# Kernel optimization log

Measured on AMD Instinct MI355X. Metric: run time of the kernel, lower is better.

The kernel has to match this reference:

```python
import jax, jax.numpy as jnp
from jax import lax
import numpy as np

CHANNEL_N = 16
HIDDEN = 128
INPUT_CH = 1
KSIZE = 7
STEPS = 10
EPS = 1e-5


def setup_inputs() -> dict:
    key = jax.random.key(0)
    ks = jax.random.split(key, 8)
    B, H, W = 8, 256, 256
    x = jax.random.normal(ks[0], (B, H, W, CHANNEL_N), dtype=jnp.float32)
    # stochastic fire masks, one per step (torch: bernoulli_(p=fire_rate) under no_grad)
    masks = jax.random.bernoulli(ks[1], 0.5, (STEPS, B, 1, H, W))
    # depthwise conv: groups=channel_n -> weight [C,1,K,K]
    conv_w = jax.random.normal(ks[2], (CHANNEL_N, 1, KSIZE, KSIZE), dtype=jnp.float32) * 0.05
    conv_b = jax.random.normal(ks[3], (CHANNEL_N,), dtype=jnp.float32) * 0.05
    # fc0: 1x1 conv [hidden, 2*C]
    fc0_w = jax.random.normal(ks[4], (HIDDEN, 2 * CHANNEL_N), dtype=jnp.float32) * 0.1
    fc0_b = jax.random.normal(ks[5], (HIDDEN,), dtype=jnp.float32) * 0.05
    # fc1: 1x1 conv [C - input_channels, hidden], no bias (zero-init in torch; random here)
    fc1_w = jax.random.normal(ks[6], (CHANNEL_N - INPUT_CH, HIDDEN), dtype=jnp.float32) * 0.02
    bn_gamma = jnp.ones((HIDDEN,), dtype=jnp.float32)
    bn_beta = jnp.zeros((HIDDEN,), dtype=jnp.float32)
    return {"x": x, "masks": masks, "conv_w": conv_w, "conv_b": conv_b,
            "fc0_w": fc0_w, "fc0_b": fc0_b, "fc1_w": fc1_w,
            "bn_gamma": bn_gamma, "bn_beta": bn_beta}


def _nca_forward(x, masks, conv_w, conv_b, fc0_w, fc0_b, fc1_w, bn_gamma, bn_beta):
    state = jnp.transpose(x, (0, 3, 1, 2))  # b h w c -> b c h w
    const_in = state[:, :INPUT_CH]
    pad = (KSIZE - 1) // 2

    def step(state, mask):
        # depthwise 7x7 conv, reflect padding
        sp = jnp.pad(state, ((0, 0), (0, 0), (pad, pad), (pad, pad)), mode='reflect')
        d = lax.conv_general_dilated(
            sp, conv_w, window_strides=(1, 1), padding='VALID',
            dimension_numbers=('NCHW', 'OIHW', 'NCHW'),
            feature_group_count=CHANNEL_N)
        d = d + conv_b[None, :, None, None]
        cat = jnp.concatenate([state, d], axis=1)  # [B, 2C, H, W]
        # fc0 (1x1 conv)
        h = jnp.einsum('bchw,oc->bohw', cat, fc0_w) + fc0_b[None, :, None, None]
        # BatchNorm2d with batch statistics (track_running_stats=False)
        mean = jnp.mean(h, axis=(0, 2, 3), keepdims=True)
        var = jnp.var(h, axis=(0, 2, 3), keepdims=True)
        h = (h - mean) * lax.rsqrt(var + EPS)
        h = h * bn_gamma[None, :, None, None] + bn_beta[None, :, None, None]
        h = jax.nn.relu(h)
        # fc1 (1x1 conv, no bias)
        delta = jnp.einsum('bohw,ko->bkhw', h, fc1_w)  # [B, C-1, H, W]
        delta = delta * mask  # stochastic fire (broadcast over channels)
        new = state[:, INPUT_CH:] + delta
        return jnp.concatenate([const_in, new], axis=1), None

    state, _ = lax.scan(step, state, masks.astype(state.dtype))
    return jnp.transpose(state, (0, 2, 3, 1))  # b c h w -> b h w c


def reference(x, masks, conv_w, conv_b, fc0_w, fc0_b, fc1_w, bn_gamma, bn_beta):
    return _nca_forward(x, masks, conv_w, conv_b, fc0_w, fc0_b, fc1_w, bn_gamma, bn_beta)
```

## Files before the change

kernel.cpp:

```cpp
#include <hip/hip_runtime.h>

#define CH 16
#define HID 128
#define NB 8
#define NH 256
#define NW 256
#define NPX (NB*NH*NW)
#define NSTEP 10
#define STEPSTATS 2240
#define GPW 8
#define KPW 4
#define SLAB 1280

typedef __attribute__((ext_vector_type(8))) short short8v;
typedef __attribute__((ext_vector_type(4))) float f32x4;

__device__ __forceinline__ int refl(int i, int n){
    if (i < 0) i = -i;
    if (i >= n) i = 2*n - 2 - i;
    return i;
}

__device__ __forceinline__ unsigned short f2bf(float x){
    unsigned int u = __float_as_uint(x);
    u += 0x7FFFu + ((u >> 16) & 1u);
    return (unsigned short)(u >> 16);
}
__device__ __forceinline__ float bf2f(unsigned short h){
    return __uint_as_float(((unsigned int)h) << 16);
}
__device__ __forceinline__ unsigned int cvtpk(float lo, float hi){
    unsigned int r;
    asm("v_cvt_pk_bf16_f32 %0, %1, %2" : "=v"(r) : "v"(lo), "v"(hi));
    return r;
}

__global__ void k_repack(const float* __restrict__ cw, const float* __restrict__ w0,
                         float* __restrict__ wp,
                         unsigned short* __restrict__ b0h, unsigned short* __restrict__ b0l){
    int t = blockIdx.x*256 + threadIdx.x;
    if (t < 49*16){ int tap = t >> 4, c = t & 15; wp[tap*16 + c] = cw[c*49 + tap]; }
    if (t < 4096){
        int n = t >> 9, l = (t >> 3) & 63, i = t & 7;
        int o = 16*n + (l & 15), k = ((l >> 4) << 3) + i;
        float v = w0[o*32 + k];
        unsigned short hi = f2bf(v);
        b0h[t] = hi;
        b0l[t] = f2bf(v - bf2f(hi));
    }
}

__global__ void k_zero(float* __restrict__ p, int n){
    int t = blockIdx.x*256 + threadIdx.x;
    if (t < n) p[t] = 0.f;
}

struct Row { float4 e[4]; float4 o[4]; };

__device__ __forceinline__ void fma4(float4& a, float4 w, float4 v){
    a.x += w.x*v.x; a.y += w.y*v.y; a.z += w.z*v.z; a.w += w.w*v.w;
}
__device__ __forceinline__ void ldrow(Row& r, const float4* L, int row, int tx){
    #pragma unroll
    for (int k=0;k<4;++k){
        r.e[k] = L[(row*2+0)*20 + tx + k];
        r.o[k] = L[(row*2+1)*20 + tx + k];
    }
}

__global__ __launch_bounds__(256,3)
void k_conv(const float* __restrict__ st, const float* __restrict__ wp,
            const float* __restrict__ cb, float* __restrict__ dout){
    __shared__ float4 tile4[38*2*20];
    __shared__ float4 cw4s[49];
    const int b = blockIdx.z >> 2, cg = blockIdx.z & 3;
    const int y0 = blockIdx.y*32, x0 = blockIdx.x*32;
    const int t = threadIdx.x;
    const int tx = t & 15, ty = t >> 4;

    if (t < 49) cw4s[t] = *(const float4*)&wp[t*16 + cg*4];
    for (int i = t; i < 38*38; i += 256){
        int py = i / 38, px = i - py*38;
        int gy = refl(y0 + py - 3, NH);
        int gx = refl(x0 + px - 3, NW);
        float4 v = *(const float4*)&st[(((size_t)b*NH + gy)*NW + gx)*CH + cg*4];
        tile4[(py*2 + (px&1))*20 + (px>>1)] = v;
    }
    __syncthreads();

    const float4* L = tile4;
    float4 bias = *(const float4*)&cb[cg*4];
    float4 a00 = bias, a01 = bias, a10 = bias, a11 = bias;
    Row A, B;
    ldrow(A, L, 2*ty,   tx);
    ldrow(B, L, 2*ty+1, tx);

#define CSTEP(dy, RA, RB, LOADNEXT, NR) \
    { \
        _Pragma("unroll") \
        for (int dx = 0; dx < 7; ++dx){ \
            float4 w4 = cw4s[(dy)*7 + dx]; \
            float4 v00 = ((dx)&1)   ? RA.o[(dx)>>1]   : RA.e[(dx)>>1]; \
            float4 v01 = ((dx+1)&1) ? RA.o[(dx+1)>>1] : RA.e[(dx+1)>>1]; \
            float4 v10 = ((dx)&1)   ? RB.o[(dx)>>1]   : RB.e[(dx)>>1]; \
            float4 v11 = ((dx+1)&1) ? RB.o[(dx+1)>>1] : RB.e[(dx+1)>>1]; \
            fma4(a00,w4,v00); fma4(a01,w4,v01); fma4(a10,w4,v10); fma4(a11,w4,v11); \
        } \
        if (LOADNEXT) ldrow(RA, L, NR, tx); \
    }

    CSTEP(0, A, B, 1, 2*ty+2)
    CSTEP(1, B, A, 1, 2*ty+3)
    CSTEP(2, A, B, 1, 2*ty+4)
    CSTEP(3, B, A, 1, 2*ty+5)
    CSTEP(4, A, B, 1, 2*ty+6)
    CSTEP(5, B, A, 1, 2*ty+7)
    CSTEP(6, A, B, 0, 0)
#undef CSTEP

    const size_t pr = ((size_t)b*NH + (size_t)(y0 + 2*ty))*NW + (x0 + 2*tx);
    *(float4*)&dout[(pr)*CH + cg*4]        = a00;
    *(float4*)&dout[(pr+1)*CH + cg*4]      = a01;
    *(float4*)&dout[(pr+NW)*CH + cg*4]     = a10;
    *(float4*)&dout[(pr+NW+1)*CH + cg*4]   = a11;
}

__global__ __launch_bounds__(512)
void k_stats(const float* __restrict__ st, const float* __restrict__ dv,
             float* __restrict__ S){
    __shared__ float lds[8*SLAB];
    const int t = threadIdx.x, lane = t & 63, w = t >> 6;
    const int lo = lane & 15, hi = lane >> 4;
    float* slab = &lds[w*SLAB];
    const int gw = blockIdx.x*8 + w;

    short8v ones;
    {
        short ov = (lo == 0) ? (short)0x3F80 : (short)0;
        #pragma unroll
        for (int i=0;i<8;++i) ones[i] = ov;
    }
    f32x4 a00 = (f32x4){0.f,0.f,0.f,0.f};
    f32x4 a01 = a00, a11 = a00, s0 = a00, s1 = a00;

    const int lp = lane >> 3, lq = lane & 7;
    const float* lbase = (lq < 4) ? st : dv;
    const int lch = (lq & 3) * 4;
    const size_t p0 = (size_t)gw * (KPW*32);

    float4 v[4];
    #pragma unroll
    for (int j2=0;j2<4;++j2)
        v[j2] = *(const float4*)&lbase[(p0 + lp + 8*j2)*CH + lch];

    #pragma unroll
    for (int j=0;j<KPW;++j){
        #pragma unroll
        for (int j2=0;j2<4;++j2){
            int p = lp + 8*j2;
            *(float2*)&slab[p*34 + lq*4]     = make_float2(v[j2].x, v[j2].y);
            *(float2*)&slab[p*34 + lq*4 + 2] = make_float2(v[j2].z, v[j2].w);
        }
        if (j+1 < KPW){
            const size_t pn = p0 + (size_t)(j+1)*32;
            #pragma unroll
            for (int j2=0;j2<4;++j2)
                v[j2] = *(const float4*)&lbase[(pn + lp + 8*j2)*CH + lch];
        }
        short8v r0h, r0l, r1h, r1l;
        #pragma unroll
        for (int ct=0;ct<2;++ct){
            #pragma unroll
            for (int i=0;i<8;++i){
                float f = slab[(hi*8+i)*34 + ct*16 + lo];
                unsigned int u = __float_as_uint(f);
                unsigned short ah = (unsigned short)(u >> 16);
                float r = f - __uint_as_float(u & 0xFFFF0000u);
                unsigned short al = (unsigned short)(__float_as_uint(r) >> 16);
                if (ct==0){ r0h[i]=(short)ah; r0l[i]=(short)al; }
                else      { r1h[i]=(short)ah; r1l[i]=(short)al; }
            }
        }
        s0 = __builtin_amdgcn_mfma_f32_16x16x32_bf16(ones, r0h, s0, 0,0,0);
        s0 = __builtin_amdgcn_mfma_f32_16x16x32_bf16(ones, r0l, s0, 0,0,0);
        s1 = __builtin_amdgcn_mfma_f32_16x16x32_bf16(ones, r1h, s1, 0,0,0);
        s1 = __builtin_amdgcn_mfma_f32_16x16x32_bf16(ones, r1l, s1, 0,0,0);
        a00 = __builtin_amdgcn_mfma_f32_16x16x32_bf16(r0h, r0h, a00, 0,0,0);
        a00 = __builtin_amdgcn_mfma_f32_16x16x32_bf16(r0l, r0h, a00, 0,0,0);
        a00 = __builtin_amdgcn_mfma_f32_16x16x32_bf16(r0h, r0l, a00, 0,0,0);
        a11 = __builtin_amdgcn_mfma_f32_16x16x32_bf16(r1h, r1h, a11, 0,0,0);
        a11 = __builtin_amdgcn_mfma_f32_16x16x32_bf16(r1l, r1h, a11, 0,0,0);
        a11 = __builtin_amdgcn_mfma_f32_16x16x32_bf16(r1h, r1l, a11, 0,0,0);
        a01 = __builtin_amdgcn_mfma_f32_16x16x32_bf16(r0h, r1h, a01, 0,0,0);
        a01 = __builtin_amdgcn_mfma_f32_16x16x32_bf16(r0l, r1h, a01, 0,0,0);
        a01 = __builtin_amdgcn_mfma_f32_16x16x32_bf16(r0h, r1l, a01, 0,0,0);
    }

    float* red = lds;
    #pragma unroll
    for (int k=0;k<4;++k){
        red[t*20 + k]      = a00[k];
        red[t*20 + 4 + k]  = a01[k];
        red[t*20 + 8 + k]  = a11[k];
        red[t*20 + 12 + k] = s0[k];
        red[t*20 + 16 + k] = s1[k];
    }
    __syncthreads();
    if (w == 0){
        float tmp[20];
        #pragma unroll
        for (int k=0;k<20;++k){
            float s = 0.f;
            #pragma unroll
            for (int ww=0;ww<8;++ww) s += red[(lane + 64*ww)*20 + k];
            tmp[k] = s;
        }
        #pragma unroll
        for (int r=0;r<4;++r){
            atomicAdd(&S[(hi*4+r)*32 + lo],        tmp[r]);
            atomicAdd(&S[(hi*4+r)*32 + 16 + lo],   tmp[4+r]);
            atomicAdd(&S[(16+lo)*32 + hi*4 + r],   tmp[4+r]);
            atomicAdd(&S[(16+hi*4+r)*32 + 16+lo],  tmp[8+r]);
        }
        if (hi == 0){
            atomicAdd(&S[1024 + lo],      tmp[12]);
            atomicAdd(&S[1024 + 16 + lo], tmp[16]);
        }
    }
}

__global__ void k_finalize(const float* __restrict__ S,
                           const float* __restrict__ w0, const float* __restrict__ b0,
                           const float* __restrict__ gam, const float* __restrict__ bet,
                           const float* __restrict__ f1, float* __restrict__ Sout){
    int o = threadIdx.x;
    const float inv = 1.f / (float)NPX;
    float w[32];
    #pragma unroll
    for (int c=0;c<32;++c) w[c] = w0[o*32+c];
    const float* su = S + 1024;
    float m1 = 0.f;
    #pragma unroll
    for (int c=0;c<32;++c) m1 += w[c]*su[c];
    m1 *= inv;
    float q = 0.f;
    for (int i=0;i<32;++i){
        float ti = 0.f;
        #pragma unroll
        for (int j=0;j<32;++j) ti += S[i*32+j]*w[j];
        q += w[i]*ti;
    }
    q *= inv;
    float var = q - m1*m1;
    float rstd = rsqrtf(var + 1e-5f);
    float mean = m1 + b0[o];
    float scale = rstd * gam[o];
    Sout[1056 + o] = bet[o]/scale + b0[o] - mean;
    unsigned short* f1sh = (unsigned short*)(Sout + 1184);
    const int base = (o>>5)*512 + ((o>>3)&3)*128 + (o&7);
    f1sh[base] = 0;
    #pragma unroll
    for (int c=1;c<16;++c)
        f1sh[base + c*8] = f2bf(f1[(c-1)*HID + o] * scale);
}

__global__ __launch_bounds__(256)
void k_update(const float* __restrict__ st, const float* __restrict__ dv,
              const int* __restrict__ msk,
              const unsigned short* __restrict__ gb0h, const unsigned short* __restrict__ gb0l,
              const float* __restrict__ Sstep, float* __restrict__ out){
    __shared__ __align__(16) unsigned int hls[4*16*68];
    const int lane = threadIdx.x & 63, w = threadIdx.x >> 6;
    const int lo16 = lane & 15, qw = lane >> 4;
    unsigned int* hb = &hls[w*16*68];

    const short8v* p0h = (const short8v*)gb0h;
    const short8v* p0l = (const short8v*)gb0l;
    const short8v* p1h = (const short8v*)(Sstep + 1184);
    short8v B0h[8], B0l[8], B1h[4];
    #pragma unroll
    for (int n=0;n<8;++n){ B0h[n] = p0h[n*64 + lane]; B0l[n] = p0l[n*64 + lane]; }
    #pragma unroll
    for (int tt=0;tt<4;++tt) B1h[tt] = p1h[tt*64 + lane];
    const float* shb = Sstep + 1056;
    float4 shbv[8];
    #pragma unroll
    for (int n=0;n<8;++n) shbv[n] = *(const float4*)&shb[16*n + 4*qw];

    const int gw = blockIdx.x*4 + w;
    const float* abase = (qw < 2) ? st : dv;
    const int choff = (qw & 1)*8;

    for (int gi = 0; gi < GPW; ++gi){
        const size_t pg0 = ((size_t)gw*GPW + gi)*16;
        const float* ap = abase + (pg0 + lo16)*CH + choff;
        float4 v0 = *(const float4*)ap;
        float4 v1 = *(const float4*)(ap + 4);
        float av[8] = {v0.x,v0.y,v0.z,v0.w,v1.x,v1.y,v1.z,v1.w};
        short8v ah, al;
        #pragma unroll
        for (int i=0;i<8;++i){
            unsigned int u = __float_as_uint(av[i]);
            ah[i] = (short)(unsigned short)(u >> 16);
            float r = av[i] - __uint_as_float(u & 0xFFFF0000u);
            al[i] = (short)(unsigned short)(__float_as_uint(r) >> 16);
        }
        f32x4 acc[8];
        #pragma unroll
        for (int n=0;n<8;++n)
            acc[n] = (f32x4){shbv[n].x, shbv[n].y, shbv[n].z, shbv[n].w};
        #pragma unroll
        for (int n=0;n<8;++n){
            acc[n] = __builtin_amdgcn_mfma_f32_16x16x32_bf16(B0h[n], ah, acc[n], 0,0,0);
            acc[n] = __builtin_amdgcn_mfma_f32_16x16x32_bf16(B0h[n], al, acc[n], 0,0,0);
            acc[n] = __builtin_amdgcn_mfma_f32_16x16x32_bf16(B0l[n], ah, acc[n], 0,0,0);
        }
        #pragma unroll
        for (int n=0;n<8;++n){
            float h0 = fmaxf(acc[n][0], 0.f), h1 = fmaxf(acc[n][1], 0.f);
            float h2 = fmaxf(acc[n][2], 0.f), h3 = fmaxf(acc[n][3], 0.f);
            unsigned int wa = cvtpk(h0, h1), wb = cvtpk(h2, h3);
            *(uint2*)&hb[lo16*68 + 8*n + 2*qw] = make_uint2(wa, wb);
        }
        f32x4 dacc = (f32x4){0.f,0.f,0.f,0.f};
        #pragma unroll
        for (int tt=0;tt<4;++tt){
            short8v ah2 = *(const short8v*)&hb[lo16*68 + 16*tt + 4*qw];
            dacc = __builtin_amdgcn_mfma_f32_16x16x32_bf16(B1h[tt], ah2, dacc, 0,0,0);
        }
        const size_t p = pg0 + lo16;
        float4 stv = *(const float4*)&st[p*CH + 4*qw];
        const float m = (float)msk[p];
        float4 ov;
        ov.x = stv.x + dacc[0]*m;
        ov.y = stv.y + dacc[1]*m;
        ov.z = stv.z + dacc[2]*m;
        ov.w = stv.w + dacc[3]*m;
        *(float4*)&out[p*CH + 4*qw] = ov;
    }
}

extern "C" void kernel_launch(void* const* d_in, const int* in_sizes, int n_in,
                              void* d_out, int out_size, void* d_ws, size_t ws_size,
                              hipStream_t stream){
    const float* x   = (const float*)d_in[0];
    const int*   mk  = (const int*)d_in[1];
    const float* cw  = (const float*)d_in[2];
    const float* cb  = (const float*)d_in[3];
    const float* w0  = (const float*)d_in[4];
    const float* b0  = (const float*)d_in[5];
    const float* f1  = (const float*)d_in[6];
    const float* gam = (const float*)d_in[7];
    const float* bet = (const float*)d_in[8];

    float* ws    = (float*)d_ws;
    float* dbuf  = ws;
    float* sbuf  = ws + (size_t)NPX*CH;
    float* stats = ws + (size_t)2*NPX*CH;
    float* wp    = stats + NSTEP*STEPSTATS;
    unsigned short* b0h = (unsigned short*)(wp + 800);
    unsigned short* b0l = b0h + 4096;

    k_repack<<<16,256,0,stream>>>(cw, w0, wp, b0h, b0l);
    k_zero<<<(NSTEP*STEPSTATS+255)/256,256,0,stream>>>(stats, NSTEP*STEPSTATS);

    const float* cur = x;
    float* outp = (float*)d_out;
    for (int s=0;s<NSTEP;++s){
        float* S = stats + (size_t)s*STEPSTATS;
        float* nxt = (s & 1) ? outp : sbuf;
        k_conv<<<dim3(NW/32,NH/32,NB*4),256,0,stream>>>(cur, wp, cb, dbuf);
        k_stats<<<512,512,0,stream>>>(cur, dbuf, S);
        k_finalize<<<1,128,0,stream>>>(S, w0, b0, gam, bet, f1, S);
        k_update<<<NPX/16/4/GPW,256,0,stream>>>(cur, dbuf, mk + (size_t)s*NPX,
                                                b0h, b0l, S, nxt);
        cur = nxt;
    }
}
```

Baseline: 1.085 ms.

## Spread BN stats atomics over 64 partial buffers and double stats grid

The stats kernel now launches twice as many blocks, each handling half as many pixel chunks, and issues all loads up front instead of software-pipelining them. Each block adds into one of 64 partial copies of the Gram/sum buffer rather than a single global one, and the redundant symmetric off-diagonal atomics are dropped. The finalize kernel first reduces the 64 partials in shared memory with 512 threads and rebuilds the symmetric block. This cuts atomic contention on the shared stats at the cost of a larger zeroing/stats buffer and an extra reduction pass.

```diff
diff --git a/kernel.cpp b/kernel.cpp
--- a/kernel.cpp
+++ b/kernel.cpp
@@ -7,10 +7,13 @@
 #define NW 256
 #define NPX (NB*NH*NW)
 #define NSTEP 10
-#define STEPSTATS 2240
 #define GPW 8
-#define KPW 4
+#define KPW 2
 #define SLAB 1280
+#define NPART 64
+#define PSTR 1088
+#define POFF (NPART*PSTR)
+#define STEPSTATS (POFF + 640)
 
 typedef __attribute__((ext_vector_type(8))) short short8v;
 typedef __attribute__((ext_vector_type(4))) float f32x4;
@@ -148,24 +151,20 @@
     const int lch = (lq & 3) * 4;
     const size_t p0 = (size_t)gw * (KPW*32);
 
-    float4 v[4];
-    #pragma unroll
-    for (int j2=0;j2<4;++j2)
-        v[j2] = *(const float4*)&lbase[(p0 + lp + 8*j2)*CH + lch];
+    float4 v[KPW][4];
+    #pragma unroll
+    for (int j=0;j<KPW;++j)
+        #pragma unroll
+        for (int j2=0;j2<4;++j2)
+            v[j][j2] = *(const float4*)&lbase[(p0 + j*32 + lp + 8*j2)*CH + lch];
 
     #pragma unroll
     for (int j=0;j<KPW;++j){
         #pragma unroll
         for (int j2=0;j2<4;++j2){
             int p = lp + 8*j2;
-            *(float2*)&slab[p*34 + lq*4]     = make_float2(v[j2].x, v[j2].y);
-            *(float2*)&slab[p*34 + lq*4 + 2] = make_float2(v[j2].z, v[j2].w);
-        }
-        if (j+1 < KPW){
-            const size_t pn = p0 + (size_t)(j+1)*32;
-            #pragma unroll
-            for (int j2=0;j2<4;++j2)
-                v[j2] = *(const float4*)&lbase[(pn + lp + 8*j2)*CH + lch];
+            *(float2*)&slab[p*34 + lq*4]     = make_float2(v[j][j2].x, v[j][j2].y);
+            *(float2*)&slab[p*34 + lq*4 + 2] = make_float2(v[j][j2].z, v[j][j2].w);
         }
         short8v r0h, r0l, r1h, r1l;
         #pragma unroll
@@ -215,53 +214,67 @@
             for (int ww=0;ww<8;++ww) s += red[(lane + 64*ww)*20 + k];
             tmp[k] = s;
         }
+        float* part = S + (size_t)(blockIdx.x & (NPART-1))*PSTR;
         #pragma unroll
         for (int r=0;r<4;++r){
-            atomicAdd(&S[(hi*4+r)*32 + lo],        tmp[r]);
-            atomicAdd(&S[(hi*4+r)*32 + 16 + lo],   tmp[4+r]);
-            atomicAdd(&S[(16+lo)*32 + hi*4 + r],   tmp[4+r]);
-            atomicAdd(&S[(16+hi*4+r)*32 + 16+lo],  tmp[8+r]);
+            atomicAdd(&part[(hi*4+r)*32 + lo],        tmp[r]);
+            atomicAdd(&part[(hi*4+r)*32 + 16 + lo],   tmp[4+r]);
+            atomicAdd(&part[(16+hi*4+r)*32 + 16+lo],  tmp[8+r]);
         }
         if (hi == 0){
-            atomicAdd(&S[1024 + lo],      tmp[12]);
-            atomicAdd(&S[1024 + 16 + lo], tmp[16]);
-        }
-    }
-}
-
-__global__ void k_finalize(const float* __restrict__ S,
+            atomicAdd(&part[1024 + lo],      tmp[12]);
+            atomicAdd(&part[1024 + 16 + lo], tmp[16]);
+        }
+    }
+}
+
+__global__ void k_finalize(const float* __restrict__ Sin,
                            const float* __restrict__ w0, const float* __restrict__ b0,
                            const float* __restrict__ gam, const float* __restrict__ bet,
                            const float* __restrict__ f1, float* __restrict__ Sout){
-    int o = threadIdx.x;
-    const float inv = 1.f / (float)NPX;
-    float w[32];
-    #pragma unroll
-    for (int c=0;c<32;++c) w[c] = w0[o*32+c];
-    const float* su = S + 1024;
-    float m1 = 0.f;
-    #pragma unroll
-    for (int c=0;c<32;++c) m1 += w[c]*su[c];
-    m1 *= inv;
-    float q = 0.f;
-    for (int i=0;i<32;++i){
-        float ti = 0.f;
-        #pragma unroll
-        for (int j=0;j<32;++j) ti += S[i*32+j]*w[j];
-        q += w[i]*ti;
-    }
-    q *= inv;
-    float var = q - m1*m1;
-    float rstd = rsqrtf(var + 1e-5f);
-    float mean = m1 + b0[o];
-    float scale = rstd * gam[o];
-    Sout[1056 + o] = bet[o]/scale + b0[o] - mean;
-    unsigned short* f1sh = (unsigned short*)(Sout + 1184);
-    const int base = (o>>5)*512 + ((o>>3)&3)*128 + (o&7);
-    f1sh[base] = 0;
-    #pragma unroll
-    for (int c=1;c<16;++c)
-        f1sh[base + c*8] = f2bf(f1[(c-1)*HID + o] * scale);
+    __shared__ float Ssm[1056];
+    const int t = threadIdx.x;
+    for (int e = t; e < 1056; e += 512){
+        float s = 0.f;
+        #pragma unroll 4
+        for (int p = 0; p < NPART; ++p) s += Sin[(size_t)p*PSTR + e];
+        Ssm[e] = s;
+    }
+    __syncthreads();
+    if (t < 128){
+        const int o = t;
+        const float inv = 1.f / (float)NPX;
+        float w[32];
+        #pragma unroll
+        for (int c=0;c<32;++c) w[c] = w0[o*32+c];
+        float m1 = 0.f;
+        #pragma unroll
+        for (int c=0;c<32;++c) m1 += w[c]*Ssm[1024+c];
+        m1 *= inv;
+        float q = 0.f;
+        #pragma unroll
+        for (int i=0;i<32;++i){
+            float ti = 0.f;
+            #pragma unroll
+            for (int j=0;j<32;++j){
+                float sv = (i >= 16 && j < 16) ? Ssm[j*32+i] : Ssm[i*32+j];
+                ti += sv*w[j];
+            }
+            q += w[i]*ti;
+        }
+        q *= inv;
+        float var = q - m1*m1;
+        float rstd = rsqrtf(var + 1e-5f);
+        float mean = m1 + b0[o];
+        float scale = rstd * gam[o];
+        Sout[POFF + o] = bet[o]/scale + b0[o] - mean;
+        unsigned short* f1sh = (unsigned short*)(Sout + POFF + 128);
+        const int base = (o>>5)*512 + ((o>>3)&3)*128 + (o&7);
+        f1sh[base] = 0;
+        #pragma unroll
+        for (int c=1;c<16;++c)
+            f1sh[base + c*8] = f2bf(f1[(c-1)*HID + o] * scale);
+    }
 }
 
 __global__ __launch_bounds__(256)
@@ -276,13 +289,13 @@
 
     const short8v* p0h = (const short8v*)gb0h;
     const short8v* p0l = (const short8v*)gb0l;
-    const short8v* p1h = (const short8v*)(Sstep + 1184);
+    const short8v* p1h = (const short8v*)(Sstep + POFF + 128);
     short8v B0h[8], B0l[8], B1h[4];
     #pragma unroll
     for (int n=0;n<8;++n){ B0h[n] = p0h[n*64 + lane]; B0l[n] = p0l[n*64 + lane]; }
     #pragma unroll
     for (int tt=0;tt<4;++tt) B1h[tt] = p1h[tt*64 + lane];
-    const float* shb = Sstep + 1056;
+    const float* shb = Sstep + POFF;
     float4 shbv[8];
     #pragma unroll
     for (int n=0;n<8;++n) shbv[n] = *(const float4*)&shb[16*n + 4*qw];
@@ -357,7 +370,7 @@
     float* dbuf  = ws;
     float* sbuf  = ws + (size_t)NPX*CH;
     float* stats = ws + (size_t)2*NPX*CH;
-    float* wp    = stats + NSTEP*STEPSTATS;
+    float* wp    = stats + (size_t)NSTEP*STEPSTATS;
     unsigned short* b0h = (unsigned short*)(wp + 800);
     unsigned short* b0l = b0h + 4096;
 
@@ -370,8 +383,8 @@
         float* S = stats + (size_t)s*STEPSTATS;
         float* nxt = (s & 1) ? outp : sbuf;
         k_conv<<<dim3(NW/32,NH/32,NB*4),256,0,stream>>>(cur, wp, cb, dbuf);
-        k_stats<<<512,512,0,stream>>>(cur, dbuf, S);
-        k_finalize<<<1,128,0,stream>>>(S, w0, b0, gam, bet, f1, S);
+        k_stats<<<1024,512,0,stream>>>(cur, dbuf, S);
+        k_finalize<<<1,512,0,stream>>>(S, w0, b0, gam, bet, f1, S);
         k_update<<<NPX/16/4/GPW,256,0,stream>>>(cur, dbuf, mk + (size_t)s*NPX,
                                                 b0h, b0l, S, nxt);
         cur = nxt;
```

Result: no change. 1.095 ms (+0.9%).
